# Kernel optimization log

Hardware: AMD Instinct MI355X
Metric: run time of the kernel (lower is better)

Reference implementation:

```python
import jax, jax.numpy as jnp
import numpy as np

B, C, L = 8, 256, 2048
D = C // 8  # q/k channel dim = 32


def setup_inputs() -> dict:
    key = jax.random.key(0)
    kx, kq, kk, kv, kg = jax.random.split(key, 5)
    kq1, kq2 = jax.random.split(kq)
    kk1, kk2 = jax.random.split(kk)
    kv1, kv2 = jax.random.split(kv)
    s = 0.05
    return {
        "x": jax.random.normal(kx, (B, C, L), dtype=jnp.float32),
        "Wq": jax.random.normal(kq1, (D, C), dtype=jnp.float32) * s,
        "bq": jax.random.normal(kq2, (D,), dtype=jnp.float32) * s,
        "Wk": jax.random.normal(kk1, (D, C), dtype=jnp.float32) * s,
        "bk": jax.random.normal(kk2, (D,), dtype=jnp.float32) * s,
        "Wv": jax.random.normal(kv1, (C, C), dtype=jnp.float32) * s,
        "bv": jax.random.normal(kv2, (C,), dtype=jnp.float32) * s,
        "gamma": jax.random.normal(kg, (1,), dtype=jnp.float32) * 0.1,
    }


def reference(x, Wq, bq, Wk, bk, Wv, bv, gamma):
    # 1x1 Conv1d == per-position channel matmul
    Q = jnp.einsum("dc,bcl->bld", Wq, x) + bq            # (B, L, D)
    K = jnp.einsum("dc,bcl->bdl", Wk, x) + bk[:, None]   # (B, D, L)
    V = jnp.einsum("oc,bcl->bol", Wv, x) + bv[:, None]   # (B, C, L)
    scale = jnp.float32(1.0 / np.sqrt(D))
    # attn[b, i, j]: softmax over j (keys)
    attn = jax.nn.softmax(jnp.einsum("bid,bdj->bij", Q, K) * scale, axis=-1)
    # out = V @ attn^T : out[b, c, i] = sum_j V[b, c, j] * attn[b, i, j]
    out = jnp.einsum("bcj,bij->bci", V, attn)            # (B, C, L)
    return gamma * out + x
```

## Files before the change

### kernel.cpp

```cpp
#include <hip/hip_runtime.h>
#include <stdint.h>


#define BB 8
#define CC 256
#define LL 2048
#define DD 32

typedef unsigned short u16;
typedef __attribute__((ext_vector_type(8))) short short8;
typedef __attribute__((ext_vector_type(4))) float f32x4;

#define SCALE_LOG2E 0.2550348612f

static __device__ __forceinline__ uint32_t pack2bf16(float hi, float lo) {
    return (__float_as_uint(hi) & 0xFFFF0000u) | (__float_as_uint(lo) >> 16);
}

static __device__ __forceinline__ float fexp2(float v) {
#if __has_builtin(__builtin_amdgcn_exp2f)
    return __builtin_amdgcn_exp2f(v);
#else
    return exp2f(v);
#endif
}

static __device__ __forceinline__ float frcp(float v) {
#if __has_builtin(__builtin_amdgcn_rcpf)
    return __builtin_amdgcn_rcpf(v);
#else
    return 1.0f / v;
#endif
}

__global__ __launch_bounds__(256) void prep_w_kernel(
    const float* __restrict__ Wq, const float* __restrict__ Wk,
    const float* __restrict__ Wv, u16* __restrict__ Wh)
{
    int idx = blockIdx.x * 256 + threadIdx.x;
    int r = idx >> 6;
    int c4 = (idx & 63) << 2;
    const float* src;
    if (r < 32)       src = Wq + (size_t)r * CC + c4;
    else if (r < 64)  src = Wk + (size_t)(r - 32) * CC + c4;
    else              src = Wv + (size_t)(r - 64) * CC + c4;
    float4 v = *(const float4*)src;
    uint2 o;
    o.x = pack2bf16(v.y, v.x);
    o.y = pack2bf16(v.w, v.z);
    *(uint2*)(Wh + (size_t)r * CC + c4) = o;
}

__global__ __launch_bounds__(256, 1) void proj_kernel(
    const float* __restrict__ x, const u16* __restrict__ Wh,
    const float* __restrict__ bq, const float* __restrict__ bk,
    const float* __restrict__ bv,
    u16* __restrict__ Qh, u16* __restrict__ Kth, u16* __restrict__ Vh)
{
    const int blk = blockIdx.x;
    const int b = blk & 7;
    const int l0 = (blk >> 3) << 6;
    const int tid = threadIdx.x;
    const int w = tid >> 6;
    const int lane = tid & 63;
    const int ln = lane & 15;
    const int q = lane >> 4;
    const int lcol = l0 + w * 16 + ln;

    const float* xb = x + (size_t)b * CC * LL;

    f32x4 acc[20];
#pragma unroll
    for (int i = 0; i < 20; ++i) acc[i] = (f32x4){0.f, 0.f, 0.f, 0.f};

    for (int c0 = 0; c0 < CC; c0 += 32) {
        const float* xp = xb + (size_t)(c0 + q * 8) * LL + lcol;
        float f[8];
#pragma unroll
        for (int e = 0; e < 8; ++e) f[e] = xp[(size_t)e * LL];
        union { uint32_t u[4]; short8 s; } bf;
#pragma unroll
        for (int d = 0; d < 4; ++d) bf.u[d] = pack2bf16(f[2 * d + 1], f[2 * d]);

#pragma unroll
        for (int mt = 0; mt < 20; ++mt) {
            const short8 af = *(const short8*)(Wh + (size_t)(mt * 16 + ln) * CC + c0 + q * 8);
            acc[mt] = __builtin_amdgcn_mfma_f32_16x16x32_bf16(af, bf.s, acc[mt], 0, 0, 0);
        }
    }

#pragma unroll
    for (int mt = 0; mt < 20; ++mt) {
        const int tbase = mt * 16;
        const int rq = tbase + q * 4;
        if (tbase < 32) {
            float v0 = (acc[mt][0] + bq[rq + 0]) * SCALE_LOG2E;
            float v1 = (acc[mt][1] + bq[rq + 1]) * SCALE_LOG2E;
            float v2 = (acc[mt][2] + bq[rq + 2]) * SCALE_LOG2E;
            float v3 = (acc[mt][3] + bq[rq + 3]) * SCALE_LOG2E;
            uint2 o; o.x = pack2bf16(v1, v0); o.y = pack2bf16(v3, v2);
            *(uint2*)(Qh + (size_t)(b * LL + lcol) * DD + rq) = o;
        } else if (tbase < 64) {
            const int rk = rq - 32;
            float v0 = acc[mt][0] + bk[rk + 0];
            float v1 = acc[mt][1] + bk[rk + 1];
            float v2 = acc[mt][2] + bk[rk + 2];
            float v3 = acc[mt][3] + bk[rk + 3];
            uint2 o; o.x = pack2bf16(v1, v0); o.y = pack2bf16(v3, v2);
            *(uint2*)(Kth + (size_t)(b * LL + lcol) * DD + rk) = o;
        } else {
            const int cv = rq - 64;
#pragma unroll
            for (int rr = 0; rr < 4; ++rr) {
                float v = acc[mt][rr] + bv[cv + rr];
                Vh[(size_t)(b * CC + cv + rr) * LL + lcol] = (u16)(__float_as_uint(v) >> 16);
            }
        }
    }
}

__global__ __launch_bounds__(256, 1) void attn_kernel(
    const u16* __restrict__ Qh, const u16* __restrict__ Kth,
    const u16* __restrict__ Vh, const float* __restrict__ x,
    const float* __restrict__ gamma, float* __restrict__ out)
{
    __shared__ u16 pbuf[4 * 64 * 40];
    const int blk = blockIdx.x;
    const int b = blk & 7;
    const int i0 = (blk >> 3) << 6;
    const int tid = threadIdx.x;
    const int w = tid >> 6;
    const int lane = tid & 63;
    const int ln = lane & 15;
    const int q = lane >> 4;

    u16* pb = pbuf + w * (64 * 40);

    short8 qf[4];
#pragma unroll
    for (int nt = 0; nt < 4; ++nt)
        qf[nt] = *(const short8*)(Qh + (size_t)(b * LL + i0 + nt * 16 + ln) * DD + q * 8);

    union { uint32_t u[4]; short8 s; } onesu;
    onesu.u[0] = onesu.u[1] = onesu.u[2] = onesu.u[3] = 0x3F803F80u;
    const short8 ones = onesu.s;

    const f32x4 zf = {0.f, 0.f, 0.f, 0.f};
    f32x4 oacc[4][4];
#pragma unroll
    for (int a = 0; a < 4; ++a)
#pragma unroll
        for (int c = 0; c < 4; ++c) oacc[a][c] = zf;
    f32x4 lacc[4];
#pragma unroll
    for (int a = 0; a < 4; ++a) lacc[a] = zf;

    const u16* Kb = Kth + (size_t)b * LL * DD;
    const u16* Vb = Vh + (size_t)(b * CC + w * 64) * LL;

    short8 kf[2], vf[4];
#pragma unroll
    for (int mt = 0; mt < 2; ++mt)
        kf[mt] = *(const short8*)(Kb + (size_t)(mt * 16 + ln) * DD + q * 8);
#pragma unroll
    for (int mt = 0; mt < 4; ++mt)
        vf[mt] = *(const short8*)(Vb + (size_t)(mt * 16 + ln) * LL + q * 8);

    for (int j0 = 0; j0 < LL; j0 += 32) {
        const int jn = (j0 + 32 < LL) ? (j0 + 32) : 0;
        short8 kn[2], vn[4];
#pragma unroll
        for (int mt = 0; mt < 2; ++mt)
            kn[mt] = *(const short8*)(Kb + (size_t)(jn + mt * 16 + ln) * DD + q * 8);
#pragma unroll
        for (int mt = 0; mt < 4; ++mt)
            vn[mt] = *(const short8*)(Vb + (size_t)(mt * 16 + ln) * LL + jn + q * 8);

        f32x4 st[2][4];
#pragma unroll
        for (int mt = 0; mt < 2; ++mt)
#pragma unroll
            for (int nt = 0; nt < 4; ++nt)
                st[mt][nt] = __builtin_amdgcn_mfma_f32_16x16x32_bf16(kf[mt], qf[nt], zf, 0, 0, 0);

#pragma unroll
        for (int mt = 0; mt < 2; ++mt)
#pragma unroll
            for (int nt = 0; nt < 4; ++nt) {
                const f32x4 sv = st[mt][nt];
                const float e0 = fexp2(sv[0]);
                const float e1 = fexp2(sv[1]);
                const float e2 = fexp2(sv[2]);
                const float e3 = fexp2(sv[3]);
                const int off = (nt * 16 + ln) * 40 + mt * 16 + q * 4;
                uint2 d; d.x = pack2bf16(e1, e0); d.y = pack2bf16(e3, e2);
                *(uint2*)(pb + off) = d;
            }

        short8 pf[4];
#pragma unroll
        for (int nt = 0; nt < 4; ++nt)
            pf[nt] = *(const short8*)(pb + (nt * 16 + ln) * 40 + q * 8);

#pragma unroll
        for (int mt = 0; mt < 4; ++mt)
#pragma unroll
            for (int nt = 0; nt < 4; ++nt)
                oacc[mt][nt] = __builtin_amdgcn_mfma_f32_16x16x32_bf16(vf[mt], pf[nt], oacc[mt][nt], 0, 0, 0);
#pragma unroll
        for (int nt = 0; nt < 4; ++nt)
            lacc[nt] = __builtin_amdgcn_mfma_f32_16x16x32_bf16(ones, pf[nt], lacc[nt], 0, 0, 0);

#pragma unroll
        for (int mt = 0; mt < 2; ++mt) kf[mt] = kn[mt];
#pragma unroll
        for (int mt = 0; mt < 4; ++mt) vf[mt] = vn[mt];
    }

    const float g = gamma[0];
    float linv[4];
#pragma unroll
    for (int nt = 0; nt < 4; ++nt) linv[nt] = frcp(lacc[nt][0]);

#pragma unroll
    for (int mt = 0; mt < 4; ++mt)
#pragma unroll
        for (int nt = 0; nt < 4; ++nt) {
            const int i = i0 + nt * 16 + ln;
#pragma unroll
            for (int r = 0; r < 4; ++r) {
                const int c = w * 64 + mt * 16 + q * 4 + r;
                const size_t idx = (size_t)(b * CC + c) * LL + i;
                out[idx] = g * (oacc[mt][nt][r] * linv[nt]) + x[idx];
            }
        }
}

extern "C" void kernel_launch(void* const* d_in, const int* in_sizes, int n_in,
                              void* d_out, int out_size, void* d_ws, size_t ws_size,
                              hipStream_t stream)
{
    const float* x     = (const float*)d_in[0];
    const float* Wq    = (const float*)d_in[1];
    const float* bq    = (const float*)d_in[2];
    const float* Wk    = (const float*)d_in[3];
    const float* bk    = (const float*)d_in[4];
    const float* Wv    = (const float*)d_in[5];
    const float* bv    = (const float*)d_in[6];
    const float* gamma = (const float*)d_in[7];
    float* out = (float*)d_out;

    uint8_t* ws = (uint8_t*)d_ws;
    u16* Wh  = (u16*)(ws + 0x000000);
    u16* Qh  = (u16*)(ws + 0x040000);
    u16* Kth = (u16*)(ws + 0x140000);
    u16* Vh  = (u16*)(ws + 0x240000);

    prep_w_kernel<<<80, 256, 0, stream>>>(Wq, Wk, Wv, Wh);
    proj_kernel<<<256, 256, 0, stream>>>(x, Wh, bq, bk, bv, Qh, Kth, Vh);
    attn_kernel<<<256, 256, 0, stream>>>(Qh, Kth, Vh, x, gamma, out);
}
```

Before: 167.2 us.

## Split attention over key halves and waves, stage score tiles, reduce via LDS

Both kernels move to 1024 threads per block. The projection kernel stages an x tile in LDS and splits the 20 output tiles across wave groups. The attention kernel splits the key range into two halves and has only channel-group-0 waves compute exp-scores into a double-buffered LDS tile that all waves reuse. This removes the fourfold redundant QK and exp work and adds intra-CU parallelism. The partial outputs and row sums are then reduced through LDS, and the epilogue stores and x reads become coalesced float4s. The cost is a __syncthreads each iteration, larger LDS use, and score work limited to a quarter of the waves.

```diff
diff --git a/kernel.cpp b/kernel.cpp
--- a/kernel.cpp
+++ b/kernel.cpp
@@ -51,12 +51,13 @@
     *(uint2*)(Wh + (size_t)r * CC + c4) = o;
 }
 
-__global__ __launch_bounds__(256, 1) void proj_kernel(
+__global__ __launch_bounds__(1024, 4) void proj_kernel(
     const float* __restrict__ x, const u16* __restrict__ Wh,
     const float* __restrict__ bq, const float* __restrict__ bk,
     const float* __restrict__ bv,
     u16* __restrict__ Qh, u16* __restrict__ Kth, u16* __restrict__ Vh)
 {
+    __shared__ float xs[256 * 68];
     const int blk = blockIdx.x;
     const int b = blk & 7;
     const int l0 = (blk >> 3) << 6;
@@ -65,66 +66,80 @@
     const int lane = tid & 63;
     const int ln = lane & 15;
     const int q = lane >> 4;
-    const int lcol = l0 + w * 16 + ln;
-
-    const float* xb = x + (size_t)b * CC * LL;
-
-    f32x4 acc[20];
-#pragma unroll
-    for (int i = 0; i < 20; ++i) acc[i] = (f32x4){0.f, 0.f, 0.f, 0.f};
+
+    const float* xb = x + (size_t)b * CC * LL + l0;
+#pragma unroll
+    for (int rr = 0; rr < 4; ++rr) {
+        const int c = w * 16 + rr * 4 + q;
+        const int l4 = ln * 4;
+        *(float4*)&xs[c * 68 + l4] = *(const float4*)(xb + (size_t)c * LL + l4);
+    }
+    __syncthreads();
+
+    const int wl = w & 3;
+    const int wm = w >> 2;
+    const int lcol = l0 + wl * 16 + ln;
+
+    f32x4 acc[5];
+#pragma unroll
+    for (int i = 0; i < 5; ++i) acc[i] = (f32x4){0.f, 0.f, 0.f, 0.f};
 
     for (int c0 = 0; c0 < CC; c0 += 32) {
-        const float* xp = xb + (size_t)(c0 + q * 8) * LL + lcol;
         float f[8];
 #pragma unroll
-        for (int e = 0; e < 8; ++e) f[e] = xp[(size_t)e * LL];
+        for (int e = 0; e < 8; ++e) f[e] = xs[(c0 + q * 8 + e) * 68 + wl * 16 + ln];
         union { uint32_t u[4]; short8 s; } bf;
 #pragma unroll
         for (int d = 0; d < 4; ++d) bf.u[d] = pack2bf16(f[2 * d + 1], f[2 * d]);
 
 #pragma unroll
-        for (int mt = 0; mt < 20; ++mt) {
+        for (int mi = 0; mi < 5; ++mi) {
+            const int mt = wm * 5 + mi;
             const short8 af = *(const short8*)(Wh + (size_t)(mt * 16 + ln) * CC + c0 + q * 8);
-            acc[mt] = __builtin_amdgcn_mfma_f32_16x16x32_bf16(af, bf.s, acc[mt], 0, 0, 0);
-        }
-    }
-
-#pragma unroll
-    for (int mt = 0; mt < 20; ++mt) {
+            acc[mi] = __builtin_amdgcn_mfma_f32_16x16x32_bf16(af, bf.s, acc[mi], 0, 0, 0);
+        }
+    }
+
+#pragma unroll
+    for (int mi = 0; mi < 5; ++mi) {
+        const int mt = wm * 5 + mi;
         const int tbase = mt * 16;
         const int rq = tbase + q * 4;
         if (tbase < 32) {
-            float v0 = (acc[mt][0] + bq[rq + 0]) * SCALE_LOG2E;
-            float v1 = (acc[mt][1] + bq[rq + 1]) * SCALE_LOG2E;
-            float v2 = (acc[mt][2] + bq[rq + 2]) * SCALE_LOG2E;
-            float v3 = (acc[mt][3] + bq[rq + 3]) * SCALE_LOG2E;
+            float v0 = (acc[mi][0] + bq[rq + 0]) * SCALE_LOG2E;
+            float v1 = (acc[mi][1] + bq[rq + 1]) * SCALE_LOG2E;
+            float v2 = (acc[mi][2] + bq[rq + 2]) * SCALE_LOG2E;
+            float v3 = (acc[mi][3] + bq[rq + 3]) * SCALE_LOG2E;
             uint2 o; o.x = pack2bf16(v1, v0); o.y = pack2bf16(v3, v2);
             *(uint2*)(Qh + (size_t)(b * LL + lcol) * DD + rq) = o;
         } else if (tbase < 64) {
             const int rk = rq - 32;
-            float v0 = acc[mt][0] + bk[rk + 0];
-            float v1 = acc[mt][1] + bk[rk + 1];
-            float v2 = acc[mt][2] + bk[rk + 2];
-            float v3 = acc[mt][3] + bk[rk + 3];
+            float v0 = acc[mi][0] + bk[rk + 0];
+            float v1 = acc[mi][1] + bk[rk + 1];
+            float v2 = acc[mi][2] + bk[rk + 2];
+            float v3 = acc[mi][3] + bk[rk + 3];
             uint2 o; o.x = pack2bf16(v1, v0); o.y = pack2bf16(v3, v2);
             *(uint2*)(Kth + (size_t)(b * LL + lcol) * DD + rk) = o;
         } else {
             const int cv = rq - 64;
 #pragma unroll
             for (int rr = 0; rr < 4; ++rr) {
-                float v = acc[mt][rr] + bv[cv + rr];
+                float v = acc[mi][rr] + bv[cv + rr];
                 Vh[(size_t)(b * CC + cv + rr) * LL + lcol] = (u16)(__float_as_uint(v) >> 16);
             }
         }
     }
 }
 
-__global__ __launch_bounds__(256, 1) void attn_kernel(
+__global__ __launch_bounds__(1024, 4) void attn_kernel(
     const u16* __restrict__ Qh, const u16* __restrict__ Kth,
     const u16* __restrict__ Vh, const float* __restrict__ x,
     const float* __restrict__ gamma, float* __restrict__ out)
 {
-    __shared__ u16 pbuf[4 * 64 * 40];
+    __shared__ u16 pbuf[2 * 4 * 32 * 40];
+    __shared__ float obuf[256 * 68];
+    __shared__ float lbuf[2 * 64];
+
     const int blk = blockIdx.x;
     const int b = blk & 7;
     const int i0 = (blk >> 3) << 6;
@@ -133,107 +148,150 @@
     const int lane = tid & 63;
     const int ln = lane & 15;
     const int q = lane >> 4;
-
-    u16* pb = pbuf + w * (64 * 40);
-
-    short8 qf[4];
-#pragma unroll
-    for (int nt = 0; nt < 4; ++nt)
-        qf[nt] = *(const short8*)(Qh + (size_t)(b * LL + i0 + nt * 16 + ln) * DD + q * 8);
+    const int wc = w >> 2;
+    const int wj = (w >> 1) & 1;
+    const int wi = w & 1;
+    const bool is_s = (wc == 0);
+
+    const u16* Kb = Kth + (size_t)b * LL * DD;
+    const u16* Vb = Vh + ((size_t)b * CC + wc * 64) * LL;
+    const int jbase = wj * 1024;
+    const int pslot = (wj * 2 + wi) * 32 * 40;
+
+    short8 qf[2];
+    if (is_s) {
+#pragma unroll
+        for (int nt = 0; nt < 2; ++nt)
+            qf[nt] = *(const short8*)(Qh + ((size_t)(b * LL) + i0 + wi * 32 + nt * 16 + ln) * DD + q * 8);
+    }
 
     union { uint32_t u[4]; short8 s; } onesu;
     onesu.u[0] = onesu.u[1] = onesu.u[2] = onesu.u[3] = 0x3F803F80u;
     const short8 ones = onesu.s;
-
     const f32x4 zf = {0.f, 0.f, 0.f, 0.f};
-    f32x4 oacc[4][4];
+
+    f32x4 oacc[4][2];
 #pragma unroll
     for (int a = 0; a < 4; ++a)
 #pragma unroll
-        for (int c = 0; c < 4; ++c) oacc[a][c] = zf;
-    f32x4 lacc[4];
-#pragma unroll
-    for (int a = 0; a < 4; ++a) lacc[a] = zf;
-
-    const u16* Kb = Kth + (size_t)b * LL * DD;
-    const u16* Vb = Vh + (size_t)(b * CC + w * 64) * LL;
-
-    short8 kf[2], vf[4];
-#pragma unroll
-    for (int mt = 0; mt < 2; ++mt)
-        kf[mt] = *(const short8*)(Kb + (size_t)(mt * 16 + ln) * DD + q * 8);
+        for (int c = 0; c < 2; ++c) oacc[a][c] = zf;
+    f32x4 lacc[2];
+    lacc[0] = zf; lacc[1] = zf;
+
+    if (is_s) {
+        u16* pw = pbuf + pslot;
+#pragma unroll
+        for (int mt = 0; mt < 2; ++mt) {
+            const short8 kf = *(const short8*)(Kb + ((size_t)(jbase + mt * 16 + ln)) * DD + q * 8);
+#pragma unroll
+            for (int nt = 0; nt < 2; ++nt) {
+                const f32x4 st = __builtin_amdgcn_mfma_f32_16x16x32_bf16(kf, qf[nt], zf, 0, 0, 0);
+                const float e0 = fexp2(st[0]), e1 = fexp2(st[1]);
+                const float e2 = fexp2(st[2]), e3 = fexp2(st[3]);
+                uint2 d; d.x = pack2bf16(e1, e0); d.y = pack2bf16(e3, e2);
+                *(uint2*)(pw + (nt * 16 + ln) * 40 + mt * 16 + q * 4) = d;
+            }
+        }
+    }
+    short8 vf[4];
 #pragma unroll
     for (int mt = 0; mt < 4; ++mt)
-        vf[mt] = *(const short8*)(Vb + (size_t)(mt * 16 + ln) * LL + q * 8);
-
-    for (int j0 = 0; j0 < LL; j0 += 32) {
-        const int jn = (j0 + 32 < LL) ? (j0 + 32) : 0;
-        short8 kn[2], vn[4];
-#pragma unroll
-        for (int mt = 0; mt < 2; ++mt)
-            kn[mt] = *(const short8*)(Kb + (size_t)(jn + mt * 16 + ln) * DD + q * 8);
+        vf[mt] = *(const short8*)(Vb + (size_t)(mt * 16 + ln) * LL + jbase + q * 8);
+    __syncthreads();
+
+    for (int it = 0; it < 32; ++it) {
+        const int cur = it & 1;
+        const int jn = jbase + ((it + 1) & 31) * 32;
+        short8 vn[4];
 #pragma unroll
         for (int mt = 0; mt < 4; ++mt)
             vn[mt] = *(const short8*)(Vb + (size_t)(mt * 16 + ln) * LL + jn + q * 8);
-
-        f32x4 st[2][4];
-#pragma unroll
-        for (int mt = 0; mt < 2; ++mt)
-#pragma unroll
-            for (int nt = 0; nt < 4; ++nt)
-                st[mt][nt] = __builtin_amdgcn_mfma_f32_16x16x32_bf16(kf[mt], qf[nt], zf, 0, 0, 0);
-
-#pragma unroll
-        for (int mt = 0; mt < 2; ++mt)
-#pragma unroll
-            for (int nt = 0; nt < 4; ++nt) {
-                const f32x4 sv = st[mt][nt];
-                const float e0 = fexp2(sv[0]);
-                const float e1 = fexp2(sv[1]);
-                const float e2 = fexp2(sv[2]);
-                const float e3 = fexp2(sv[3]);
-                const int off = (nt * 16 + ln) * 40 + mt * 16 + q * 4;
-                uint2 d; d.x = pack2bf16(e1, e0); d.y = pack2bf16(e3, e2);
-                *(uint2*)(pb + off) = d;
+        short8 kn[2];
+        if (is_s && (it + 1 < 32)) {
+#pragma unroll
+            for (int mt = 0; mt < 2; ++mt)
+                kn[mt] = *(const short8*)(Kb + ((size_t)(jn + mt * 16 + ln)) * DD + q * 8);
+        }
+        const u16* pr = pbuf + cur * (4 * 32 * 40) + pslot;
+        short8 pf[2];
+#pragma unroll
+        for (int nt = 0; nt < 2; ++nt)
+            pf[nt] = *(const short8*)(pr + (nt * 16 + ln) * 40 + q * 8);
+#pragma unroll
+        for (int mt = 0; mt < 4; ++mt)
+#pragma unroll
+            for (int nt = 0; nt < 2; ++nt)
+                oacc[mt][nt] = __builtin_amdgcn_mfma_f32_16x16x32_bf16(vf[mt], pf[nt], oacc[mt][nt], 0, 0, 0);
+        if (is_s) {
+#pragma unroll
+            for (int nt = 0; nt < 2; ++nt)
+                lacc[nt] = __builtin_amdgcn_mfma_f32_16x16x32_bf16(ones, pf[nt], lacc[nt], 0, 0, 0);
+            if (it + 1 < 32) {
+                u16* pw = pbuf + (1 - cur) * (4 * 32 * 40) + pslot;
+#pragma unroll
+                for (int mt = 0; mt < 2; ++mt) {
+#pragma unroll
+                    for (int nt = 0; nt < 2; ++nt) {
+                        const f32x4 st = __builtin_amdgcn_mfma_f32_16x16x32_bf16(kn[mt], qf[nt], zf, 0, 0, 0);
+                        const float e0 = fexp2(st[0]), e1 = fexp2(st[1]);
+                        const float e2 = fexp2(st[2]), e3 = fexp2(st[3]);
+                        uint2 d; d.x = pack2bf16(e1, e0); d.y = pack2bf16(e3, e2);
+                        *(uint2*)(pw + (nt * 16 + ln) * 40 + mt * 16 + q * 4) = d;
+                    }
+                }
             }
-
-        short8 pf[4];
-#pragma unroll
-        for (int nt = 0; nt < 4; ++nt)
-            pf[nt] = *(const short8*)(pb + (nt * 16 + ln) * 40 + q * 8);
-
+        }
+#pragma unroll
+        for (int mt = 0; mt < 4; ++mt) vf[mt] = vn[mt];
+        __syncthreads();
+    }
+
+    if (is_s && q == 0) {
+#pragma unroll
+        for (int nt = 0; nt < 2; ++nt)
+            lbuf[wj * 64 + wi * 32 + nt * 16 + ln] = lacc[nt][0];
+    }
+    if (wj == 0) {
 #pragma unroll
         for (int mt = 0; mt < 4; ++mt)
 #pragma unroll
-            for (int nt = 0; nt < 4; ++nt)
-                oacc[mt][nt] = __builtin_amdgcn_mfma_f32_16x16x32_bf16(vf[mt], pf[nt], oacc[mt][nt], 0, 0, 0);
-#pragma unroll
-        for (int nt = 0; nt < 4; ++nt)
-            lacc[nt] = __builtin_amdgcn_mfma_f32_16x16x32_bf16(ones, pf[nt], lacc[nt], 0, 0, 0);
-
-#pragma unroll
-        for (int mt = 0; mt < 2; ++mt) kf[mt] = kn[mt];
-#pragma unroll
-        for (int mt = 0; mt < 4; ++mt) vf[mt] = vn[mt];
-    }
+            for (int nt = 0; nt < 2; ++nt)
+#pragma unroll
+                for (int r = 0; r < 4; ++r)
+                    obuf[(wc * 64 + mt * 16 + q * 4 + r) * 68 + wi * 32 + nt * 16 + ln] = oacc[mt][nt][r];
+    }
+    __syncthreads();
+    if (wj == 1) {
+#pragma unroll
+        for (int mt = 0; mt < 4; ++mt)
+#pragma unroll
+            for (int nt = 0; nt < 2; ++nt)
+#pragma unroll
+                for (int r = 0; r < 4; ++r)
+                    obuf[(wc * 64 + mt * 16 + q * 4 + r) * 68 + wi * 32 + nt * 16 + ln] += oacc[mt][nt][r];
+    }
+    __syncthreads();
 
     const float g = gamma[0];
-    float linv[4];
-#pragma unroll
-    for (int nt = 0; nt < 4; ++nt) linv[nt] = frcp(lacc[nt][0]);
-
-#pragma unroll
-    for (int mt = 0; mt < 4; ++mt)
-#pragma unroll
-        for (int nt = 0; nt < 4; ++nt) {
-            const int i = i0 + nt * 16 + ln;
-#pragma unroll
-            for (int r = 0; r < 4; ++r) {
-                const int c = w * 64 + mt * 16 + q * 4 + r;
-                const size_t idx = (size_t)(b * CC + c) * LL + i;
-                out[idx] = g * (oacc[mt][nt][r] * linv[nt]) + x[idx];
-            }
-        }
+    const int il = (tid & 15) * 4;
+    const float4 la = *(const float4*)&lbuf[il];
+    const float4 lb2 = *(const float4*)&lbuf[64 + il];
+    float4 li;
+    li.x = frcp(la.x + lb2.x); li.y = frcp(la.y + lb2.y);
+    li.z = frcp(la.z + lb2.z); li.w = frcp(la.w + lb2.w);
+#pragma unroll
+    for (int rr = 0; rr < 4; ++rr) {
+        const int c = (tid >> 4) + rr * 64;
+        const float4 ov = *(const float4*)&obuf[c * 68 + il];
+        const size_t idx = ((size_t)b * CC + c) * LL + i0 + il;
+        const float4 xv = *(const float4*)(x + idx);
+        float4 o;
+        o.x = g * (ov.x * li.x) + xv.x;
+        o.y = g * (ov.y * li.y) + xv.y;
+        o.z = g * (ov.z * li.z) + xv.z;
+        o.w = g * (ov.w * li.w) + xv.w;
+        *(float4*)(out + idx) = o;
+    }
 }
 
 extern "C" void kernel_launch(void* const* d_in, const int* in_sizes, int n_in,
@@ -257,6 +315,6 @@
     u16* Vh  = (u16*)(ws + 0x240000);
 
     prep_w_kernel<<<80, 256, 0, stream>>>(Wq, Wk, Wv, Wh);
-    proj_kernel<<<256, 256, 0, stream>>>(x, Wh, bq, bk, bv, Qh, Kth, Vh);
-    attn_kernel<<<256, 256, 0, stream>>>(Qh, Kth, Vh, x, gamma, out);
-}
+    proj_kernel<<<256, 1024, 0, stream>>>(x, Wh, bq, bk, bv, Qh, Kth, Vh);
+    attn_kernel<<<256, 1024, 0, stream>>>(Qh, Kth, Vh, x, gamma, out);
+}
```

Result: no change. 170.1 us (+1.7%).

## Transpose x to bf16, split projection finer, share P tile across 8 waves

Applied to the files above, without the earlier changes.

Adds a kernel that transposes x into position-major bf16 so the projection kernel reads contiguous 16-byte rows. The projection grid is split four ways across output rows, so each wave holds 5 accumulators instead of 20 and more blocks can be resident. The attention kernel now uses 512 threads: each wave computes scores for its own key slice into a shared 64x256 P tile, then all waves multiply it against their 32 V channels. Row sums are accumulated in registers and reduced through shared memory instead of using a ones-MFMA. The change adds an extra kernel launch, an extra round trip of x through memory, and two barriers per key chunk.

```diff
diff --git a/kernel.cpp b/kernel.cpp
--- a/kernel.cpp
+++ b/kernel.cpp
@@ -51,80 +51,115 @@
     *(uint2*)(Wh + (size_t)r * CC + c4) = o;
 }
 
-__global__ __launch_bounds__(256, 1) void proj_kernel(
-    const float* __restrict__ x, const u16* __restrict__ Wh,
+__global__ __launch_bounds__(256) void prep_xt_kernel(
+    const float* __restrict__ x, u16* __restrict__ xt)
+{
+    __shared__ float xs[64 * 65];
+    const int blk = blockIdx.x;
+    const int b = blk & 7;
+    const int t = blk >> 3;
+    const int l0 = (t & 31) << 6;
+    const int c0 = (t >> 5) << 6;
+    const int tid = threadIdx.x;
+    const int ln16 = tid & 15;
+    const int r0 = tid >> 4;
+
+    const float* xb = x + ((size_t)(b * CC + c0)) * LL + l0;
+#pragma unroll
+    for (int rr = 0; rr < 4; ++rr) {
+        const int c = r0 + rr * 16;
+        const float4 v = *(const float4*)(xb + (size_t)c * LL + ln16 * 4);
+        float* d = &xs[c * 65 + ln16 * 4];
+        d[0] = v.x; d[1] = v.y; d[2] = v.z; d[3] = v.w;
+    }
+    __syncthreads();
+    u16* xo = xt + ((size_t)(b * LL + l0)) * CC + c0;
+    const int c4 = ln16 * 4;
+#pragma unroll
+    for (int rr = 0; rr < 4; ++rr) {
+        const int l = r0 + rr * 16;
+        const float f0 = xs[(c4 + 0) * 65 + l];
+        const float f1 = xs[(c4 + 1) * 65 + l];
+        const float f2 = xs[(c4 + 2) * 65 + l];
+        const float f3 = xs[(c4 + 3) * 65 + l];
+        uint2 o; o.x = pack2bf16(f1, f0); o.y = pack2bf16(f3, f2);
+        *(uint2*)(xo + (size_t)l * CC + c4) = o;
+    }
+}
+
+__global__ __launch_bounds__(256, 4) void proj_kernel(
+    const u16* __restrict__ xt, const u16* __restrict__ Wh,
     const float* __restrict__ bq, const float* __restrict__ bk,
     const float* __restrict__ bv,
     u16* __restrict__ Qh, u16* __restrict__ Kth, u16* __restrict__ Vh)
 {
     const int blk = blockIdx.x;
     const int b = blk & 7;
-    const int l0 = (blk >> 3) << 6;
+    const int t = blk >> 3;
+    const int l0 = (t & 63) << 5;
+    const int mh = t >> 6;
     const int tid = threadIdx.x;
     const int w = tid >> 6;
     const int lane = tid & 63;
     const int ln = lane & 15;
     const int q = lane >> 4;
-    const int lcol = l0 + w * 16 + ln;
-
-    const float* xb = x + (size_t)b * CC * LL;
-
-    f32x4 acc[20];
-#pragma unroll
-    for (int i = 0; i < 20; ++i) acc[i] = (f32x4){0.f, 0.f, 0.f, 0.f};
-
+    const int wl = w & 1;
+    const int wm = w >> 1;
+    const int l = l0 + wl * 16 + ln;
+    const u16* xrow = xt + ((size_t)(b * LL) + l) * CC;
+    const int mbase = mh * 160 + wm * 80;
+
+    f32x4 acc[5];
+#pragma unroll
+    for (int i = 0; i < 5; ++i) acc[i] = (f32x4){0.f, 0.f, 0.f, 0.f};
+
+#pragma unroll
     for (int c0 = 0; c0 < CC; c0 += 32) {
-        const float* xp = xb + (size_t)(c0 + q * 8) * LL + lcol;
-        float f[8];
-#pragma unroll
-        for (int e = 0; e < 8; ++e) f[e] = xp[(size_t)e * LL];
-        union { uint32_t u[4]; short8 s; } bf;
-#pragma unroll
-        for (int d = 0; d < 4; ++d) bf.u[d] = pack2bf16(f[2 * d + 1], f[2 * d]);
-
-#pragma unroll
-        for (int mt = 0; mt < 20; ++mt) {
-            const short8 af = *(const short8*)(Wh + (size_t)(mt * 16 + ln) * CC + c0 + q * 8);
-            acc[mt] = __builtin_amdgcn_mfma_f32_16x16x32_bf16(af, bf.s, acc[mt], 0, 0, 0);
-        }
-    }
-
-#pragma unroll
-    for (int mt = 0; mt < 20; ++mt) {
-        const int tbase = mt * 16;
-        const int rq = tbase + q * 4;
-        if (tbase < 32) {
-            float v0 = (acc[mt][0] + bq[rq + 0]) * SCALE_LOG2E;
-            float v1 = (acc[mt][1] + bq[rq + 1]) * SCALE_LOG2E;
-            float v2 = (acc[mt][2] + bq[rq + 2]) * SCALE_LOG2E;
-            float v3 = (acc[mt][3] + bq[rq + 3]) * SCALE_LOG2E;
+        const short8 bf = *(const short8*)(xrow + c0 + q * 8);
+#pragma unroll
+        for (int mt = 0; mt < 5; ++mt) {
+            const short8 af = *(const short8*)(Wh + (size_t)(mbase + mt * 16 + ln) * CC + c0 + q * 8);
+            acc[mt] = __builtin_amdgcn_mfma_f32_16x16x32_bf16(af, bf, acc[mt], 0, 0, 0);
+        }
+    }
+
+#pragma unroll
+    for (int mt = 0; mt < 5; ++mt) {
+        const int rg = mbase + mt * 16 + q * 4;
+        if (rg < 32) {
+            float v0 = (acc[mt][0] + bq[rg + 0]) * SCALE_LOG2E;
+            float v1 = (acc[mt][1] + bq[rg + 1]) * SCALE_LOG2E;
+            float v2 = (acc[mt][2] + bq[rg + 2]) * SCALE_LOG2E;
+            float v3 = (acc[mt][3] + bq[rg + 3]) * SCALE_LOG2E;
             uint2 o; o.x = pack2bf16(v1, v0); o.y = pack2bf16(v3, v2);
-            *(uint2*)(Qh + (size_t)(b * LL + lcol) * DD + rq) = o;
-        } else if (tbase < 64) {
-            const int rk = rq - 32;
+            *(uint2*)(Qh + ((size_t)(b * LL) + l) * DD + rg) = o;
+        } else if (rg < 64) {
+            const int rk = rg - 32;
             float v0 = acc[mt][0] + bk[rk + 0];
             float v1 = acc[mt][1] + bk[rk + 1];
             float v2 = acc[mt][2] + bk[rk + 2];
             float v3 = acc[mt][3] + bk[rk + 3];
             uint2 o; o.x = pack2bf16(v1, v0); o.y = pack2bf16(v3, v2);
-            *(uint2*)(Kth + (size_t)(b * LL + lcol) * DD + rk) = o;
+            *(uint2*)(Kth + ((size_t)(b * LL) + l) * DD + rk) = o;
         } else {
-            const int cv = rq - 64;
+            const int cv = rg - 64;
 #pragma unroll
             for (int rr = 0; rr < 4; ++rr) {
-                float v = acc[mt][rr] + bv[cv + rr];
-                Vh[(size_t)(b * CC + cv + rr) * LL + lcol] = (u16)(__float_as_uint(v) >> 16);
-            }
-        }
-    }
-}
-
-__global__ __launch_bounds__(256, 1) void attn_kernel(
+                const float v = acc[mt][rr] + bv[cv + rr];
+                Vh[((size_t)(b * CC) + cv + rr) * LL + l] = (u16)(__float_as_uint(v) >> 16);
+            }
+        }
+    }
+}
+
+__global__ __launch_bounds__(512, 2) void attn_kernel(
     const u16* __restrict__ Qh, const u16* __restrict__ Kth,
     const u16* __restrict__ Vh, const float* __restrict__ x,
     const float* __restrict__ gamma, float* __restrict__ out)
 {
-    __shared__ u16 pbuf[4 * 64 * 40];
+    __shared__ u16 pbuf[64 * 264];
+    __shared__ float lbuf[8 * 64];
+
     const int blk = blockIdx.x;
     const int b = blk & 7;
     const int i0 = (blk >> 3) << 6;
@@ -134,106 +169,96 @@
     const int ln = lane & 15;
     const int q = lane >> 4;
 
-    u16* pb = pbuf + w * (64 * 40);
+    const u16* Qb = Qh + ((size_t)(b * LL) + i0) * DD;
+    const u16* Kb = Kth + (size_t)(b * LL) * DD;
+    const u16* Vb = Vh + ((size_t)(b * CC) + w * 32) * LL;
 
     short8 qf[4];
 #pragma unroll
-    for (int nt = 0; nt < 4; ++nt)
-        qf[nt] = *(const short8*)(Qh + (size_t)(b * LL + i0 + nt * 16 + ln) * DD + q * 8);
-
-    union { uint32_t u[4]; short8 s; } onesu;
-    onesu.u[0] = onesu.u[1] = onesu.u[2] = onesu.u[3] = 0x3F803F80u;
-    const short8 ones = onesu.s;
+    for (int it = 0; it < 4; ++it)
+        qf[it] = *(const short8*)(Qb + (size_t)(it * 16 + ln) * DD + q * 8);
 
     const f32x4 zf = {0.f, 0.f, 0.f, 0.f};
-    f32x4 oacc[4][4];
-#pragma unroll
-    for (int a = 0; a < 4; ++a)
+    f32x4 oacc[2][4];
+#pragma unroll
+    for (int a = 0; a < 2; ++a)
 #pragma unroll
         for (int c = 0; c < 4; ++c) oacc[a][c] = zf;
-    f32x4 lacc[4];
-#pragma unroll
-    for (int a = 0; a < 4; ++a) lacc[a] = zf;
-
-    const u16* Kb = Kth + (size_t)b * LL * DD;
-    const u16* Vb = Vh + (size_t)(b * CC + w * 64) * LL;
-
-    short8 kf[2], vf[4];
-#pragma unroll
-    for (int mt = 0; mt < 2; ++mt)
-        kf[mt] = *(const short8*)(Kb + (size_t)(mt * 16 + ln) * DD + q * 8);
-#pragma unroll
-    for (int mt = 0; mt < 4; ++mt)
-        vf[mt] = *(const short8*)(Vb + (size_t)(mt * 16 + ln) * LL + q * 8);
-
-    for (int j0 = 0; j0 < LL; j0 += 32) {
-        const int jn = (j0 + 32 < LL) ? (j0 + 32) : 0;
-        short8 kn[2], vn[4];
-#pragma unroll
-        for (int mt = 0; mt < 2; ++mt)
-            kn[mt] = *(const short8*)(Kb + (size_t)(jn + mt * 16 + ln) * DD + q * 8);
-#pragma unroll
-        for (int mt = 0; mt < 4; ++mt)
-            vn[mt] = *(const short8*)(Vb + (size_t)(mt * 16 + ln) * LL + jn + q * 8);
-
-        f32x4 st[2][4];
-#pragma unroll
-        for (int mt = 0; mt < 2; ++mt)
-#pragma unroll
-            for (int nt = 0; nt < 4; ++nt)
-                st[mt][nt] = __builtin_amdgcn_mfma_f32_16x16x32_bf16(kf[mt], qf[nt], zf, 0, 0, 0);
-
-#pragma unroll
-        for (int mt = 0; mt < 2; ++mt)
-#pragma unroll
-            for (int nt = 0; nt < 4; ++nt) {
-                const f32x4 sv = st[mt][nt];
-                const float e0 = fexp2(sv[0]);
-                const float e1 = fexp2(sv[1]);
-                const float e2 = fexp2(sv[2]);
-                const float e3 = fexp2(sv[3]);
-                const int off = (nt * 16 + ln) * 40 + mt * 16 + q * 4;
+    float lsum[4] = {0.f, 0.f, 0.f, 0.f};
+
+    for (int jm = 0; jm < 8; ++jm) {
+        const int j0 = jm * 256;
+        const int js = j0 + w * 32;
+
+#pragma unroll
+        for (int jt = 0; jt < 2; ++jt) {
+            const short8 kf = *(const short8*)(Kb + (size_t)(js + jt * 16 + ln) * DD + q * 8);
+#pragma unroll
+            for (int it = 0; it < 4; ++it) {
+                const f32x4 st = __builtin_amdgcn_mfma_f32_16x16x32_bf16(kf, qf[it], zf, 0, 0, 0);
+                const float e0 = fexp2(st[0]), e1 = fexp2(st[1]);
+                const float e2 = fexp2(st[2]), e3 = fexp2(st[3]);
+                lsum[it] += (e0 + e1) + (e2 + e3);
                 uint2 d; d.x = pack2bf16(e1, e0); d.y = pack2bf16(e3, e2);
-                *(uint2*)(pb + off) = d;
-            }
-
-        short8 pf[4];
-#pragma unroll
-        for (int nt = 0; nt < 4; ++nt)
-            pf[nt] = *(const short8*)(pb + (nt * 16 + ln) * 40 + q * 8);
-
-#pragma unroll
-        for (int mt = 0; mt < 4; ++mt)
-#pragma unroll
-            for (int nt = 0; nt < 4; ++nt)
-                oacc[mt][nt] = __builtin_amdgcn_mfma_f32_16x16x32_bf16(vf[mt], pf[nt], oacc[mt][nt], 0, 0, 0);
-#pragma unroll
-        for (int nt = 0; nt < 4; ++nt)
-            lacc[nt] = __builtin_amdgcn_mfma_f32_16x16x32_bf16(ones, pf[nt], lacc[nt], 0, 0, 0);
-
-#pragma unroll
-        for (int mt = 0; mt < 2; ++mt) kf[mt] = kn[mt];
-#pragma unroll
-        for (int mt = 0; mt < 4; ++mt) vf[mt] = vn[mt];
-    }
+                *(uint2*)(&pbuf[(it * 16 + ln) * 264 + w * 32 + jt * 16 + q * 4]) = d;
+            }
+        }
+        __syncthreads();
+
+        short8 vf0 = *(const short8*)(Vb + (size_t)(ln) * LL + j0 + q * 8);
+        short8 vf1 = *(const short8*)(Vb + (size_t)(16 + ln) * LL + j0 + q * 8);
+#pragma unroll
+        for (int k = 0; k < 8; ++k) {
+            const int kn = ((k + 1) & 7) * 32;
+            const short8 vn0 = *(const short8*)(Vb + (size_t)(ln) * LL + j0 + kn + q * 8);
+            const short8 vn1 = *(const short8*)(Vb + (size_t)(16 + ln) * LL + j0 + kn + q * 8);
+#pragma unroll
+            for (int it = 0; it < 4; ++it) {
+                const short8 pf = *(const short8*)(&pbuf[(it * 16 + ln) * 264 + k * 32 + q * 8]);
+                oacc[0][it] = __builtin_amdgcn_mfma_f32_16x16x32_bf16(vf0, pf, oacc[0][it], 0, 0, 0);
+                oacc[1][it] = __builtin_amdgcn_mfma_f32_16x16x32_bf16(vf1, pf, oacc[1][it], 0, 0, 0);
+            }
+            vf0 = vn0; vf1 = vn1;
+        }
+        __syncthreads();
+    }
+
+#pragma unroll
+    for (int it = 0; it < 4; ++it) {
+        float s = lsum[it];
+        s += __shfl_xor(s, 16);
+        s += __shfl_xor(s, 32);
+        lsum[it] = s;
+    }
+    if (q == 0) {
+#pragma unroll
+        for (int it = 0; it < 4; ++it) lbuf[w * 64 + it * 16 + ln] = lsum[it];
+    }
+    __syncthreads();
 
     const float g = gamma[0];
     float linv[4];
 #pragma unroll
-    for (int nt = 0; nt < 4; ++nt) linv[nt] = frcp(lacc[nt][0]);
-
-#pragma unroll
-    for (int mt = 0; mt < 4; ++mt)
-#pragma unroll
-        for (int nt = 0; nt < 4; ++nt) {
-            const int i = i0 + nt * 16 + ln;
+    for (int it = 0; it < 4; ++it) {
+        float s = 0.f;
+#pragma unroll
+        for (int ww = 0; ww < 8; ++ww) s += lbuf[ww * 64 + it * 16 + ln];
+        linv[it] = frcp(s);
+    }
+
+#pragma unroll
+    for (int ct = 0; ct < 2; ++ct) {
+        const int c = w * 32 + ct * 16 + q * 4;
+#pragma unroll
+        for (int it = 0; it < 4; ++it) {
+            const int i = i0 + it * 16 + ln;
 #pragma unroll
             for (int r = 0; r < 4; ++r) {
-                const int c = w * 64 + mt * 16 + q * 4 + r;
-                const size_t idx = (size_t)(b * CC + c) * LL + i;
-                out[idx] = g * (oacc[mt][nt][r] * linv[nt]) + x[idx];
-            }
-        }
+                const size_t idx = ((size_t)(b * CC + c + r)) * LL + i;
+                out[idx] = g * (oacc[ct][it][r] * linv[it]) + x[idx];
+            }
+        }
+    }
 }
 
 extern "C" void kernel_launch(void* const* d_in, const int* in_sizes, int n_in,
@@ -252,11 +277,13 @@
 
     uint8_t* ws = (uint8_t*)d_ws;
     u16* Wh  = (u16*)(ws + 0x000000);
-    u16* Qh  = (u16*)(ws + 0x040000);
-    u16* Kth = (u16*)(ws + 0x140000);
-    u16* Vh  = (u16*)(ws + 0x240000);
+    u16* xt  = (u16*)(ws + 0x040000);
+    u16* Qh  = (u16*)(ws + 0x840000);
+    u16* Kth = (u16*)(ws + 0x940000);
+    u16* Vh  = (u16*)(ws + 0xA40000);
 
     prep_w_kernel<<<80, 256, 0, stream>>>(Wq, Wk, Wv, Wh);
-    proj_kernel<<<256, 256, 0, stream>>>(x, Wh, bq, bk, bv, Qh, Kth, Vh);
-    attn_kernel<<<256, 256, 0, stream>>>(Qh, Kth, Vh, x, gamma, out);
-}
+    prep_xt_kernel<<<1024, 256, 0, stream>>>(x, xt);
+    proj_kernel<<<1024, 256, 0, stream>>>(xt, Wh, bq, bk, bv, Qh, Kth, Vh);
+    attn_kernel<<<256, 512, 0, stream>>>(Qh, Kth, Vh, x, gamma, out);
+}
```

After: 157.4 us. -5.9%, faster.
